# Performance work log

Hardware: AMD Instinct MI355X
Metric: run time of the kernel (lower is better)

The kernel has to match this reference:

```python
import jax, jax.numpy as jnp
import numpy as np

N = 6144; D0 = 512; D1 = 256; D2 = 128; K = 10
ALPHA = 1.0; BETA = 1.0; P = 0.004  # edge density -> ~25 avg degree


def _xavier(key, shape):
    limit = float(np.sqrt(6.0 / (shape[0] + shape[1])))
    return jax.random.uniform(key, shape, jnp.float32, -limit, limit)


def setup_inputs() -> dict:
    key = jax.random.key(0)
    ks = jax.random.split(key, 20)

    def adj(k):
        k1, k2 = jax.random.split(k)
        u = jax.random.uniform(k1, (N, N), jnp.float32)
        w = jax.random.uniform(k2, (N, N), jnp.float32)
        return jnp.where(u < P, w, 0.0)  # sparse weighted adjacency, dense storage

    return {
        "A": adj(ks[0]), "A2": adj(ks[1]),
        "X": jax.random.normal(ks[2], (N, D0), jnp.float32),
        "X2": jax.random.normal(ks[3], (N, D0), jnp.float32),
        "W11": _xavier(ks[4], (D0, D1)), "v111": _xavier(ks[5], (D1, 1)), "v112": _xavier(ks[6], (D1, 1)),
        "W12": _xavier(ks[7], (D1, D2)), "v121": _xavier(ks[8], (D2, 1)), "v122": _xavier(ks[9], (D2, 1)),
        "W21": _xavier(ks[10], (D0, D1)), "v211": _xavier(ks[11], (D1, 1)), "v212": _xavier(ks[12], (D1, 1)),
        "W22": _xavier(ks[13], (D1, D2)), "v221": _xavier(ks[14], (D2, 1)), "v222": _xavier(ks[15], (D2, 1)),
        "mu": _xavier(ks[16], (K, D2)),
    }


def _gat(A, H, v1, v2):
    # logits_ij = A_ij * (H v1)_i + A_ij * (H v2)_j, support = nonzeros of A;
    # torch.sparse.softmax over each row of sigmoid(logits) restricted to support.
    f1 = H @ v1                       # [N,1]
    f2 = H @ v2                       # [N,1]
    logits = A * f1 + A * f2.T        # [N,N]
    mask = A != 0.0
    e = jnp.where(mask, jnp.exp(jax.nn.sigmoid(logits)), 0.0)
    denom = jnp.sum(e, axis=1, keepdims=True)
    return e / jnp.where(denom == 0.0, 1.0, denom)  # empty rows -> all-zero row


def _autoenc(A, X, layers):
    H = X
    Cs = []
    for (W, v1, v2) in layers:          # encoder
        H = H @ W
        C = _gat(A, H, v1, v2)
        Cs.append(C)
        H = C @ H
    H_enc = H
    for i in range(len(layers) - 1, -1, -1):  # decoder (tied weights, cached attention)
        H = H @ layers[i][0].T
        H = Cs[i] @ H
    return H_enc, H


def reference(A, X, A2, X2, W11, v111, v112, W12, v121, v122,
              W21, v211, v212, W22, v221, v222, mu):
    H, X_ = _autoenc(A, X, [(W11, v111, v112), (W12, v121, v122)])
    H2, X_2 = _autoenc(A2, X2, [(W21, v211, v212), (W22, v221, v222)])
    H_F = H + H2 * BETA
    # Student-t soft assignment
    d2 = jnp.sum((H_F[:, None, :] - mu[None, :, :]) ** 2, axis=2)  # [N,K]
    q = (1.0 / (1.0 + d2 / ALPHA)) ** ((ALPHA + 1.0) / 2.0)
    q = q / jnp.sum(q, axis=1, keepdims=True)
    return (H_F, q, H, H2, X_, X_2)
```

## Files before the change

kernel.cpp:

```cpp
#include <hip/hip_runtime.h>
#include <hip/hip_bf16.h>

#define NN 6144
#define CAP 128

typedef short bf8 __attribute__((ext_vector_type(8)));
typedef float f4 __attribute__((ext_vector_type(4)));

__device__ inline unsigned short f2bf(float x) {
  union { float f; unsigned u; } v; v.f = x;
  unsigned r = v.u + 0x7fff + ((v.u >> 16) & 1);
  return (unsigned short)(r >> 16);
}
__device__ inline float bf2f(unsigned short b) {
  union { float f; unsigned u; } v; v.u = ((unsigned)b) << 16;
  return v.f;
}


__device__ void dev_sparsify(int bid, int tid,
    const float* __restrict__ A0, const float* __restrict__ A1,
    int* __restrict__ colsB, float* __restrict__ valsB, int* __restrict__ cntB) {
  const int br = bid >= 1536;
  const int bb = br ? bid - 1536 : bid;
  const float* __restrict__ A = br ? A1 : A0;
  int* cols = colsB + (size_t)br * NN * CAP;
  float* vals = valsB + (size_t)br * NN * CAP;
  int* cnt = cntB + br * NN;
  int row = (bb * 256 + tid) >> 6;
  int lane = tid & 63;
  const f4* __restrict__ arow = (const f4*)(A + (size_t)row * NN);
  int base = 0;
  for (int it = 0; it < 24; it += 6) {
    f4 v[6];
#pragma unroll
    for (int u = 0; u < 6; ++u) v[u] = __builtin_nontemporal_load(&arow[(it + u) * 64 + lane]);
#pragma unroll
    for (int u = 0; u < 6; ++u) {
      float xs[4] = {v[u][0], v[u][1], v[u][2], v[u][3]};
      unsigned long long m[4];
#pragma unroll
      for (int q = 0; q < 4; ++q) m[q] = __ballot(xs[q] != 0.0f);
      int off0 = base;
      int off1 = off0 + __popcll(m[0]);
      int off2 = off1 + __popcll(m[1]);
      int off3 = off2 + __popcll(m[2]);
      base = off3 + __popcll(m[3]);
      int offs[4] = {off0, off1, off2, off3};
      unsigned long long lmask = (1ull << lane) - 1ull;
#pragma unroll
      for (int q = 0; q < 4; ++q) {
        if (xs[q] != 0.0f) {
          int idx = offs[q] + __popcll(m[q] & lmask);
          if (idx < CAP) {
            cols[row * CAP + idx] = ((it + u) * 64 + lane) * 4 + q;
            vals[row * CAP + idx] = xs[q];
          }
        }
      }
    }
  }
  if (lane == 0) cnt[row] = base < CAP ? base : CAP;
}

__device__ void dev_convw(int cb, int tid,
    const float* __restrict__ W11, const float* __restrict__ W21,
    const float* __restrict__ W12, const float* __restrict__ W22,
    short* __restrict__ W1th, short* __restrict__ W1tl,
    short* __restrict__ W2th, short* __restrict__ W2tl) {
  const int S1 = 512 * 256, S2 = 256 * 128;
  int i = cb * 256 + tid;
  if (i < 2 * S1) {
    int br = i >= S1;
    int idx = br ? i - S1 : i;
    float x = (br ? W21 : W11)[idx];
    unsigned short h = f2bf(x), l = f2bf(x - bf2f(h));
    int r = idx / 256, c = idx % 256;
    size_t o = (size_t)br * S1;
    W1th[o + c * 512 + r] = (short)h; W1tl[o + c * 512 + r] = (short)l;
  } else {
    int i2 = i - 2 * S1;
    if (i2 >= 2 * S2) return;
    int br = i2 >= S2;
    int idx = br ? i2 - S2 : i2;
    float x = (br ? W22 : W12)[idx];
    unsigned short h = f2bf(x), l = f2bf(x - bf2f(h));
    int r = idx / 128, c = idx % 128;
    size_t o = (size_t)br * S2;
    W2th[o + c * 256 + r] = (short)h; W2tl[o + c * 256 + r] = (short)l;
  }
}

__device__ void dev_convX(int xb, int tid,
    const float* __restrict__ X0, const float* __restrict__ X1,
    short* __restrict__ XhB) {
  const int br = xb >= 3072;
  const int b = br ? xb - 3072 : xb;
  const float* __restrict__ in = br ? X1 : X0;
  short* hi = XhB + (size_t)br * NN * 512;
  int i = b * 256 + tid;
  float4 v = *(const float4*)&in[i * 4];
  short4 h;
  h.x = (short)f2bf(v.x);
  h.y = (short)f2bf(v.y);
  h.z = (short)f2bf(v.z);
  h.w = (short)f2bf(v.w);
  *(short4*)&hi[i * 4] = h;
}

__device__ void dev_wc2(int wb, int tid, char* smemc,
    const float* __restrict__ W11, const float* __restrict__ W12,
    const float* __restrict__ W21, const float* __restrict__ W22,
    short* __restrict__ Wch, short* __restrict__ Wcl) {
  const int bx = wb & 7, by = (wb >> 3) & 1, br = wb >> 4;
  const float* W1 = br ? W21 : W11;
  const float* W2 = br ? W22 : W12;
  short* Ch = Wch + (size_t)br * 512 * 128;
  short* Cl = Wcl + (size_t)br * 512 * 128;
  float (*As)[68] = (float(*)[68])smemc;
  float (*Bs)[68] = (float(*)[68])(smemc + 16 * 68 * 4);
  const int bm = bx * 64, bn = by * 64;
  const int t = tid;
  const int tm = (t >> 4) * 4, tn = (t & 15) * 4;
  const int la_m = t >> 2, la_k = (t & 3) * 4;
  const int lb_k = t >> 4, lb_n = (t & 15) * 4;
  float acc[4][4] = {};
  for (int k0 = 0; k0 < 256; k0 += 16) {
    float4 a4 = *(const float4*)&W1[(size_t)(bm + la_m) * 256 + k0 + la_k];
    float4 b4 = *(const float4*)&W2[(size_t)(k0 + lb_k) * 128 + bn + lb_n];
    __syncthreads();
    As[la_k + 0][la_m] = a4.x;
    As[la_k + 1][la_m] = a4.y;
    As[la_k + 2][la_m] = a4.z;
    As[la_k + 3][la_m] = a4.w;
    Bs[lb_k][lb_n + 0] = b4.x;
    Bs[lb_k][lb_n + 1] = b4.y;
    Bs[lb_k][lb_n + 2] = b4.z;
    Bs[lb_k][lb_n + 3] = b4.w;
    __syncthreads();
#pragma unroll
    for (int k = 0; k < 16; ++k) {
      float a0 = As[k][tm + 0], a1 = As[k][tm + 1], a2 = As[k][tm + 2], a3 = As[k][tm + 3];
      float b0 = Bs[k][tn + 0], b1 = Bs[k][tn + 1], b2 = Bs[k][tn + 2], b3 = Bs[k][tn + 3];
      acc[0][0] += a0 * b0; acc[0][1] += a0 * b1; acc[0][2] += a0 * b2; acc[0][3] += a0 * b3;
      acc[1][0] += a1 * b0; acc[1][1] += a1 * b1; acc[1][2] += a1 * b2; acc[1][3] += a1 * b3;
      acc[2][0] += a2 * b0; acc[2][1] += a2 * b1; acc[2][2] += a2 * b2; acc[2][3] += a2 * b3;
      acc[3][0] += a3 * b0; acc[3][1] += a3 * b1; acc[3][2] += a3 * b2; acc[3][3] += a3 * b3;
    }
  }
#pragma unroll
  for (int i = 0; i < 4; ++i)
#pragma unroll
    for (int j = 0; j < 4; ++j) {
      float x = acc[i][j];
      size_t off = (size_t)(bm + tm + i) * 128 + bn + tn + j;
      unsigned short h = f2bf(x);
      Ch[off] = (short)h;
      Cl[off] = (short)f2bf(x - bf2f(h));
    }
}

__device__ void dev_fvec256(int fb, int tid,
    const short* __restrict__ HB, const float* __restrict__ v10,
    const float* __restrict__ v20, const float* __restrict__ v11,
    const float* __restrict__ v21, float* __restrict__ f1B, float* __restrict__ f2B) {
  const int br = fb >= 1536;
  const int bb = br ? fb - 1536 : fb;
  const short* H = HB + (size_t)br * NN * 256;
  const float* v1 = br ? v11 : v10;
  const float* v2 = br ? v21 : v20;
  float* f1 = f1B + br * NN;
  float* f2 = f2B + br * NN;
  int row = (bb * 256 + tid) >> 6;
  int lane = tid & 63;
  const short* hp = H + (size_t)row * 256 + lane * 4;
  float s1 = 0.f, s2 = 0.f;
#pragma unroll
  for (int e = 0; e < 4; ++e) {
    float h = bf2f((unsigned short)hp[e]);
    s1 += h * v1[lane * 4 + e];
    s2 += h * v2[lane * 4 + e];
  }
#pragma unroll
  for (int o = 32; o; o >>= 1) {
    s1 += __shfl_xor(s1, o);
    s2 += __shfl_xor(s2, o);
  }
  if (lane == 0) { f1[row] = s1; f2[row] = s2; }
}

#define GS 40
#define MFMA_BF16 __builtin_amdgcn_mfma_f32_16x16x32_bf16

template <bool ALO, int EPI>
__device__ void dev_gemm(int bx, int by, int br, int tid, char* smemc,
    const short* __restrict__ AhB, const short* __restrict__ AlB, size_t sA,
    const short* __restrict__ BhB, const short* __restrict__ BlB, size_t sB,
    float* __restrict__ CfB, short* __restrict__ ChB, short* __restrict__ ClB,
    size_t sC, int K, int Nn) {
  short* sAh = (short*)smemc;
  short* sBh = sAh + 64 * GS;
  short* sBl = sBh + 64 * GS;
  short* sAl = sBl + 64 * GS;
  const short* Ahg = AhB + br * sA;
  const short* Bhg = BhB + br * sB;
  const short* Blg = BlB + br * sB;
  const int bm = bx * 64, bn = by * 64;
  const int t = tid;
  const int lane = t & 63, w = t >> 6;
  const int wm = (w & 1) * 32, wn = (w >> 1) * 32;
  const int fr = lane & 15, fq = lane >> 4;
  const int srow = t >> 2, sk = (t & 3) * 8;

  f4 acc[2][2] = {};

  for (int k0 = 0; k0 < K; k0 += 32) {
    const size_t aoff = (size_t)(bm + srow) * K + k0 + sk;
    const size_t boff = (size_t)(bn + srow) * K + k0 + sk;
    bf8 vah = *(const bf8*)&Ahg[aoff];
    bf8 vbh = *(const bf8*)&Bhg[boff];
    bf8 vbl = *(const bf8*)&Blg[boff];
    bf8 val_;
    if constexpr (ALO) val_ = *(const bf8*)&(AlB + br * sA)[aoff];
    __syncthreads();
    *(bf8*)&sAh[srow * GS + sk] = vah;
    *(bf8*)&sBh[srow * GS + sk] = vbh;
    *(bf8*)&sBl[srow * GS + sk] = vbl;
    if constexpr (ALO) *(bf8*)&sAl[srow * GS + sk] = val_;
    __syncthreads();

    bf8 ah[2], al[2], bh[2], bl[2];
#pragma unroll
    for (int i = 0; i < 2; ++i) {
      ah[i] = *(bf8*)&sAh[(wm + i * 16 + fr) * GS + fq * 8];
      bh[i] = *(bf8*)&sBh[(wn + i * 16 + fr) * GS + fq * 8];
      bl[i] = *(bf8*)&sBl[(wn + i * 16 + fr) * GS + fq * 8];
      if constexpr (ALO) al[i] = *(bf8*)&sAl[(wm + i * 16 + fr) * GS + fq * 8];
    }
#pragma unroll
    for (int mi = 0; mi < 2; ++mi)
#pragma unroll
      for (int ni = 0; ni < 2; ++ni) {
        acc[mi][ni] = MFMA_BF16(ah[mi], bh[ni], acc[mi][ni], 0, 0, 0);
        acc[mi][ni] = MFMA_BF16(ah[mi], bl[ni], acc[mi][ni], 0, 0, 0);
        if constexpr (ALO) acc[mi][ni] = MFMA_BF16(al[mi], bh[ni], acc[mi][ni], 0, 0, 0);
      }
  }

  float* Cf = CfB ? CfB + br * sC : nullptr;
  short* Ch = ChB ? ChB + br * sC : nullptr;
  short* Cl = ClB ? ClB + br * sC : nullptr;
#pragma unroll
  for (int mi = 0; mi < 2; ++mi)
#pragma unroll
    for (int ni = 0; ni < 2; ++ni) {
      int cidx = bn + wn + ni * 16 + fr;
#pragma unroll
      for (int r = 0; r < 4; ++r) {
        size_t off = (size_t)(bm + wm + mi * 16 + fq * 4 + r) * Nn + cidx;
        float x = acc[mi][ni][r];
        if constexpr (EPI == 0) Cf[off] = x;
        if constexpr (EPI >= 1) {
          unsigned short h = f2bf(x);
          Ch[off] = (short)h;
          if constexpr (EPI == 2) Cl[off] = (short)f2bf(x - bf2f(h));
        }
      }
    }
}

template <bool WLO>
__device__ void dev_spmm128(int sb, int tid,
    const int* __restrict__ colsB, const float* __restrict__ cvalsB,
    const int* __restrict__ cntB, const short* __restrict__ HinB,
    short* __restrict__ HhB, short* __restrict__ HlB) {
  const int br = sb >= 1536;
  const int bb = br ? sb - 1536 : sb;
  const int* cols = colsB + (size_t)br * NN * CAP;
  const float* cvals = cvalsB + (size_t)br * NN * CAP;
  const int* cnt = cntB + br * NN;
  const short* Hin = HinB + (size_t)br * NN * 128;
  int row = (bb * 256 + tid) >> 6;
  int lane = tid & 63;
  int c = cnt[row];
  const int base = row * CAP;
  float cv0 = 0.f, cv1 = 0.f;
  int j0 = 0, j1 = 0;
  if (lane < c) { j0 = cols[base + lane]; cv0 = cvals[base + lane]; }
  if (64 + lane < c) { j1 = cols[base + 64 + lane]; cv1 = cvals[base + 64 + lane]; }
  float2 acc = make_float2(0.f, 0.f);
  for (int k = 0; k < c; k += 8) {
    unsigned hv[8]; float cv[8];
#pragma unroll
    for (int u = 0; u < 8; ++u) {
      int kk = k + u;
      if (kk < c) {
        int jj = (kk & 64) ? j1 : j0;
        float cc = (kk & 64) ? cv1 : cv0;
        int j = __shfl(jj, kk & 63);
        cv[u] = __shfl(cc, kk & 63);
        hv[u] = *(const unsigned*)&Hin[(size_t)j * 128 + lane * 2];
      }
    }
#pragma unroll
    for (int u = 0; u < 8; ++u) {
      if (k + u < c) {
        acc.x += cv[u] * bf2f((unsigned short)(hv[u] & 0xffff));
        acc.y += cv[u] * bf2f((unsigned short)(hv[u] >> 16));
      }
    }
  }
  size_t o = (size_t)br * NN * 128 + (size_t)row * 128 + lane * 2;
  unsigned short hx = f2bf(acc.x), hy = f2bf(acc.y);
  *(unsigned*)&HhB[o] = (unsigned)hx | ((unsigned)hy << 16);
  if constexpr (WLO) {
    unsigned short lx = f2bf(acc.x - bf2f(hx)), ly = f2bf(acc.y - bf2f(hy));
    *(unsigned*)&HlB[o] = (unsigned)lx | ((unsigned)ly << 16);
  }
}

__device__ void dev_final(int fb, int tid,
    const float* __restrict__ H1e, const float* __restrict__ H2e,
    const float* __restrict__ mu, float* __restrict__ hf_out,
    float* __restrict__ q_out) {
  int row = (fb * 256 + tid) >> 6;
  int lane = tid & 63;
  float2 h1 = *(const float2*)&H1e[row * 128 + lane * 2];
  float2 h2 = *(const float2*)&H2e[row * 128 + lane * 2];
  float2 hf = make_float2(h1.x + h2.x, h1.y + h2.y);
  *(float2*)&hf_out[row * 128 + lane * 2] = hf;
  float d2[10];
#pragma unroll
  for (int k = 0; k < 10; ++k) {
    float dx = hf.x - mu[k * 128 + lane * 2];
    float dy = hf.y - mu[k * 128 + lane * 2 + 1];
    d2[k] = dx * dx + dy * dy;
  }
#pragma unroll
  for (int k = 0; k < 10; ++k)
#pragma unroll
    for (int o = 32; o; o >>= 1) d2[k] += __shfl_xor(d2[k], o);
  float q[10], s = 0.f;
#pragma unroll
  for (int k = 0; k < 10; ++k) { q[k] = 1.f / (1.f + d2[k]); s += q[k]; }
  float inv = 1.f / s;
  if (lane < 10) q_out[row * 10 + lane] = q[lane] * inv;
}


__global__ __launch_bounds__(256) void k1_prep(
    const float* A0, const float* A1, int* colsB, float* valsB, int* cntB,
    const float* W11, const float* W21, const float* W12, const float* W22,
    short* W1th, short* W1tl, short* W2th, short* W2tl,
    const float* X0, const float* X1, short* XhB,
    short* Wc2h, short* Wc2l) {
  __shared__ char smem[2 * 16 * 68 * 4];
  int bid = blockIdx.x, tid = threadIdx.x;
  if (bid < 3072) dev_sparsify(bid, tid, A0, A1, colsB, valsB, cntB);
  else if (bid < 4352) dev_convw(bid - 3072, tid, W11, W21, W12, W22,
                                 W1th, W1tl, W2th, W2tl);
  else if (bid < 10496) dev_convX(bid - 4352, tid, X0, X1, XhB);
  else dev_wc2(bid - 10496, tid, smem, W11, W12, W21, W22, Wc2h, Wc2l);
}

template <bool ALO, int EPI>
__global__ __launch_bounds__(256) void gemm_nt(
    const short* AhB, const short* AlB, size_t sA,
    const short* BhB, const short* BlB, size_t sB,
    float* CfB, short* ChB, short* ClB, size_t sC, int K, int Nn) {
  __shared__ char smem[(ALO ? 4 : 3) * 64 * GS * 2];
  dev_gemm<ALO, EPI>(blockIdx.x, blockIdx.y, blockIdx.z, threadIdx.x, smem,
                     AhB, AlB, sA, BhB, BlB, sB, CfB, ChB, ClB, sC, K, Nn);
}

__global__ __launch_bounds__(256) void k3_gemm2_fvec(
    const short* H1h, const short* W2th, const short* W2tl, short* G1h,
    const float* v111, const float* v112, const float* v211, const float* v212,
    float* f1, float* f2) {
  __shared__ char smem[3 * 64 * GS * 2];
  int bid = blockIdx.x, tid = threadIdx.x;
  if (bid < 384) {
    int bx = bid % 96, r = bid / 96;
    int by = r & 1, br = r >> 1;
    dev_gemm<false, 1>(bx, by, br, tid, smem, H1h, nullptr, (size_t)NN * 256,
                       W2th, W2tl, (size_t)256 * 128, nullptr, G1h, nullptr,
                       (size_t)NN * 128, 256, 128);
  } else {
    dev_fvec256(bid - 384, tid, H1h, v111, v112, v211, v212, f1, f2);
  }
}

template <bool WF32, bool FUSE>
__global__ __launch_bounds__(256) void gatspmm_kernel(
    const int* __restrict__ colsB, const float* __restrict__ avalsB,
    const int* __restrict__ cntB, const float* __restrict__ f1B,
    const float* __restrict__ f2B, float* __restrict__ cvalsB,
    const short* __restrict__ HinB, float* __restrict__ HoutB,
    short* __restrict__ HhB,
    const float* __restrict__ nv10, const float* __restrict__ nv20,
    const float* __restrict__ nv11, const float* __restrict__ nv21,
    float* __restrict__ g1B, float* __restrict__ g2B) {
  const int br = blockIdx.y;
  const int* cols = colsB + (size_t)br * NN * CAP;
  const float* avals = avalsB + (size_t)br * NN * CAP;
  const int* cnt = cntB + br * NN;
  const float* f1 = f1B + br * NN;
  const float* f2 = f2B + br * NN;
  float* cvals = cvalsB + (size_t)br * NN * CAP;
  const short* Hin = HinB + (size_t)br * NN * 128;
  int row = (blockIdx.x * blockDim.x + threadIdx.x) >> 6;
  int lane = threadIdx.x & 63;
  int c = cnt[row];
  float f1i = f1[row];
  const int base = row * CAP;
  float e0 = 0.f, e1 = 0.f;
  int j0 = 0, j1 = 0;
  {
    int k = lane;
    if (k < c) {
      float a = avals[base + k];
      j0 = cols[base + k];
      float lg = a * (f1i + f2[j0]);
      e0 = expf(1.f / (1.f + expf(-lg)));
    }
    k = 64 + lane;
    if (k < c) {
      float a = avals[base + k];
      j1 = cols[base + k];
      float lg = a * (f1i + f2[j1]);
      e1 = expf(1.f / (1.f + expf(-lg)));
    }
  }
  float s = e0 + e1;
#pragma unroll
  for (int o = 32; o; o >>= 1) s += __shfl_xor(s, o);
  float inv = (s == 0.f) ? 1.f : 1.f / s;
  if (lane < c) cvals[base + lane] = e0 * inv;
  if (64 + lane < c) cvals[base + 64 + lane] = e1 * inv;

  float2 acc = make_float2(0.f, 0.f);
  for (int k = 0; k < c; k += 8) {
    unsigned hv[8]; float cv[8];
#pragma unroll
    for (int u = 0; u < 8; ++u) {
      int kk = k + u;
      if (kk < c) {
        int jj = (kk & 64) ? j1 : j0;
        float ee = (kk & 64) ? e1 : e0;
        int j = __shfl(jj, kk & 63);
        cv[u] = __shfl(ee, kk & 63) * inv;
        hv[u] = *(const unsigned*)&Hin[(size_t)j * 128 + lane * 2];
      }
    }
#pragma unroll
    for (int u = 0; u < 8; ++u) {
      if (k + u < c) {
        acc.x += cv[u] * bf2f((unsigned short)(hv[u] & 0xffff));
        acc.y += cv[u] * bf2f((unsigned short)(hv[u] >> 16));
      }
    }
  }
  size_t o = (size_t)br * NN * 128 + (size_t)row * 128 + lane * 2;
  if constexpr (WF32) *(float2*)&HoutB[o] = acc;
  unsigned hw = (unsigned)(unsigned short)f2bf(acc.x) | ((unsigned)f2bf(acc.y) << 16);
  *(unsigned*)&HhB[o] = hw;
  if constexpr (FUSE) {
    const float* w1 = br ? nv11 : nv10;
    const float* w2 = br ? nv21 : nv20;
    float s1 = acc.x * w1[lane * 2] + acc.y * w1[lane * 2 + 1];
    float s2 = acc.x * w2[lane * 2] + acc.y * w2[lane * 2 + 1];
#pragma unroll
    for (int o2 = 32; o2; o2 >>= 1) {
      s1 += __shfl_xor(s1, o2);
      s2 += __shfl_xor(s2, o2);
    }
    if (lane == 0) { g1B[br * NN + row] = s1; g2B[br * NN + row] = s2; }
  }
}

__global__ __launch_bounds__(256) void k6_spmm_final(
    const int* colsB, const float* c2v, const int* cntB,
    const short* Hech, short* C2sh,
    const float* H1e, const float* H2e, const float* mu,
    float* hf_out, float* q_out) {
  int bid = blockIdx.x, tid = threadIdx.x;
  if (bid < 3072) dev_spmm128<false>(bid, tid, colsB, c2v, cntB, Hech, C2sh, nullptr);
  else dev_final(bid - 3072, tid, H1e, H2e, mu, hf_out, q_out);
}

__global__ __launch_bounds__(256) void spmm128hl_kernel(
    const int* colsB, const float* cvalsB, const int* cntB,
    const short* HinB, short* HhB, short* HlB) {
  dev_spmm128<true>(blockIdx.x + blockIdx.y * 1536, threadIdx.x,
                    colsB, cvalsB, cntB, HinB, HhB, HlB);
}

extern "C" void kernel_launch(void* const* d_in, const int* in_sizes, int n_in,
                              void* d_out, int out_size, void* d_ws, size_t ws_size,
                              hipStream_t stream) {
  const int D0 = 512, D1 = 256, D2 = 128;
  const int S1 = D0 * D1, S2 = D1 * D2;
  float* out = (float*)d_out;
  const size_t o0 = 0;
  const size_t o1 = o0 + (size_t)NN * 128;
  const size_t o2 = o1 + (size_t)NN * 10;
  const size_t o3 = o2 + (size_t)NN * 128;
  const size_t o4 = o3 + (size_t)NN * 128;
  const size_t o5 = o4 + (size_t)NN * 512;

  char* w = (char*)d_ws;
  auto alloc = [&](size_t bytes) -> void* {
    void* p = (void*)w;
    w += (bytes + 255) & ~(size_t)255;
    return p;
  };
  int*   cols  = (int*)  alloc((size_t)2 * NN * CAP * 4);
  float* avals = (float*)alloc((size_t)2 * NN * CAP * 4);
  float* c1v   = (float*)alloc((size_t)2 * NN * CAP * 4);
  float* c2v   = (float*)alloc((size_t)2 * NN * CAP * 4);
  int*   cnt   = (int*)  alloc((size_t)2 * NN * 4);
  float* f1    = (float*)alloc((size_t)2 * NN * 4);
  float* f2    = (float*)alloc((size_t)2 * NN * 4);
  float* g1    = (float*)alloc((size_t)2 * NN * 4);
  float* g2    = (float*)alloc((size_t)2 * NN * 4);
  short* Xh    = (short*)alloc((size_t)2 * NN * D0 * 2);
  short* H1h   = (short*)alloc((size_t)2 * NN * D1 * 2);
  short* G1h   = (short*)alloc((size_t)2 * NN * D2 * 2);
  short* H2h   = (short*)alloc((size_t)2 * NN * D2 * 2);
  short* Hech  = (short*)alloc((size_t)2 * NN * D2 * 2);
  short* C2sh  = (short*)alloc((size_t)2 * NN * D2 * 2);
  short* Cth   = (short*)alloc((size_t)2 * NN * D2 * 2);
  short* Ctl   = (short*)alloc((size_t)2 * NN * D2 * 2);
  short* W1th  = (short*)alloc((size_t)2 * S1 * 2);
  short* W1tl  = (short*)alloc((size_t)2 * S1 * 2);
  short* W2th  = (short*)alloc((size_t)2 * S2 * 2);
  short* W2tl  = (short*)alloc((size_t)2 * S2 * 2);
  short* Wc2h  = (short*)alloc((size_t)2 * 512 * 128 * 2);
  short* Wc2l  = (short*)alloc((size_t)2 * 512 * 128 * 2);

  const float* A   = (const float*)d_in[0];
  const float* A2  = (const float*)d_in[1];
  const float* X   = (const float*)d_in[2];
  const float* X2  = (const float*)d_in[3];
  const float* W11 = (const float*)d_in[4];
  const float* v111= (const float*)d_in[5];
  const float* v112= (const float*)d_in[6];
  const float* W12 = (const float*)d_in[7];
  const float* v121= (const float*)d_in[8];
  const float* v122= (const float*)d_in[9];
  const float* W21 = (const float*)d_in[10];
  const float* v211= (const float*)d_in[11];
  const float* v212= (const float*)d_in[12];
  const float* W22 = (const float*)d_in[13];
  const float* v221= (const float*)d_in[14];
  const float* v222= (const float*)d_in[15];
  const float* mu  = (const float*)d_in[16];

  const dim3 rows2(NN / 4, 2);

  k1_prep<<<10528, 256, 0, stream>>>(
      A, A2, cols, avals, cnt, W11, W21, W12, W22,
      W1th, W1tl, W2th, W2tl, X, X2, Xh, Wc2h, Wc2l);
  gemm_nt<false, 1><<<dim3(NN / 64, D1 / 64, 2), 256, 0, stream>>>(
      Xh, nullptr, (size_t)NN * D0, W1th, W1tl, (size_t)S1,
      nullptr, H1h, nullptr, (size_t)NN * D1, D0, D1);
  k3_gemm2_fvec<<<3456, 256, 0, stream>>>(
      H1h, W2th, W2tl, G1h, v111, v112, v211, v212, f1, f2);
  gatspmm_kernel<false, true><<<rows2, 256, 0, stream>>>(
      cols, avals, cnt, f1, f2, c1v, G1h, nullptr, H2h,
      v121, v122, v221, v222, g1, g2);
  gatspmm_kernel<true, false><<<rows2, 256, 0, stream>>>(
      cols, avals, cnt, g1, g2, c2v, H2h, out + o2, Hech,
      nullptr, nullptr, nullptr, nullptr, nullptr, nullptr);
  k6_spmm_final<<<4608, 256, 0, stream>>>(
      cols, c2v, cnt, Hech, C2sh, out + o2, out + o3, mu, out + o0, out + o1);
  spmm128hl_kernel<<<rows2, 256, 0, stream>>>(cols, c1v, cnt, C2sh, Cth, Ctl);
  gemm_nt<true, 0><<<dim3(NN / 64, D0 / 64, 2), 256, 0, stream>>>(
      Cth, Ctl, (size_t)NN * D2, Wc2h, Wc2l, (size_t)(512 * 128),
      out + o4, nullptr, nullptr, (size_t)NN * D0, D2, D0);
}
```

Before: 164.3 us.

## Overlap adjacency sparsification with first GEMM and stage CSR writes via LDS

Splits the prep kernel in two. The W/X bf16 conversions run first. A second kernel then runs the adjacency sparsification, the first feature GEMM (X·W1) and the Wc2 construction as separate block ranges, so the bandwidth-bound scan of A can overlap with the compute-bound GEMM. Sparsify now builds each row's column and value lists in shared memory and writes all CAP slots with coalesced stores, replacing scattered per-lane global writes. The trade-offs are one extra launch and the copying of stale or uninitialized staging entries past each row's count into global memory.

```diff
diff --git a/kernel.cpp b/kernel.cpp
--- a/kernel.cpp
+++ b/kernel.cpp
@@ -18,7 +18,7 @@
 }
 
 
-__device__ void dev_sparsify(int bid, int tid,
+__device__ void dev_sparsify(int bid, int tid, char* smem,
     const float* __restrict__ A0, const float* __restrict__ A1,
     int* __restrict__ colsB, float* __restrict__ valsB, int* __restrict__ cntB) {
   const int br = bid >= 1536;
@@ -27,8 +27,10 @@
   int* cols = colsB + (size_t)br * NN * CAP;
   float* vals = valsB + (size_t)br * NN * CAP;
   int* cnt = cntB + br * NN;
-  int row = (bb * 256 + tid) >> 6;
-  int lane = tid & 63;
+  const int wv = tid >> 6, lane = tid & 63;
+  const int row = bb * 4 + wv;
+  int* colstage = (int*)(smem + wv * 1024);
+  float* valstage = (float*)(smem + wv * 1024 + 512);
   const f4* __restrict__ arow = (const f4*)(A + (size_t)row * NN);
   int base = 0;
   for (int it = 0; it < 24; it += 6) {
@@ -53,13 +55,21 @@
         if (xs[q] != 0.0f) {
           int idx = offs[q] + __popcll(m[q] & lmask);
           if (idx < CAP) {
-            cols[row * CAP + idx] = ((it + u) * 64 + lane) * 4 + q;
-            vals[row * CAP + idx] = xs[q];
+            colstage[idx] = ((it + u) * 64 + lane) * 4 + q;
+            valstage[idx] = xs[q];
           }
         }
       }
     }
   }
+  __syncthreads();
+  const int rbase = row * CAP;
+  int c0 = colstage[lane], c1 = colstage[64 + lane];
+  float v0 = valstage[lane], v1 = valstage[64 + lane];
+  cols[rbase + lane] = c0;
+  cols[rbase + 64 + lane] = c1;
+  vals[rbase + lane] = v0;
+  vals[rbase + 64 + lane] = v1;
   if (lane == 0) cnt[row] = base < CAP ? base : CAP;
 }
 
@@ -348,19 +358,34 @@
 }
 
 
-__global__ __launch_bounds__(256) void k1_prep(
-    const float* A0, const float* A1, int* colsB, float* valsB, int* cntB,
+__global__ __launch_bounds__(256) void k0_prep(
     const float* W11, const float* W21, const float* W12, const float* W22,
     short* W1th, short* W1tl, short* W2th, short* W2tl,
-    const float* X0, const float* X1, short* XhB,
+    const float* X0, const float* X1, short* XhB) {
+  int bid = blockIdx.x, tid = threadIdx.x;
+  if (bid < 1280) dev_convw(bid, tid, W11, W21, W12, W22, W1th, W1tl, W2th, W2tl);
+  else dev_convX(bid - 1280, tid, X0, X1, XhB);
+}
+
+__global__ __launch_bounds__(256) void k1_main(
+    const float* A0, const float* A1, int* colsB, float* valsB, int* cntB,
+    const short* Xh, const short* W1th, const short* W1tl, short* H1h,
+    const float* W11, const float* W12, const float* W21, const float* W22,
     short* Wc2h, short* Wc2l) {
-  __shared__ char smem[2 * 16 * 68 * 4];
+  __shared__ char smem[15360];
   int bid = blockIdx.x, tid = threadIdx.x;
-  if (bid < 3072) dev_sparsify(bid, tid, A0, A1, colsB, valsB, cntB);
-  else if (bid < 4352) dev_convw(bid - 3072, tid, W11, W21, W12, W22,
-                                 W1th, W1tl, W2th, W2tl);
-  else if (bid < 10496) dev_convX(bid - 4352, tid, X0, X1, XhB);
-  else dev_wc2(bid - 10496, tid, smem, W11, W12, W21, W22, Wc2h, Wc2l);
+  if (bid < 3072) {
+    dev_sparsify(bid, tid, smem, A0, A1, colsB, valsB, cntB);
+  } else if (bid < 3840) {
+    int g = bid - 3072;
+    int bx = g % 96, r = g / 96;
+    int by = r & 3, brz = r >> 2;
+    dev_gemm<false, 1>(bx, by, brz, tid, smem, Xh, nullptr, (size_t)NN * 512,
+                       W1th, W1tl, (size_t)512 * 256, nullptr, H1h, nullptr,
+                       (size_t)NN * 256, 512, 256);
+  } else {
+    dev_wc2(bid - 3840, tid, smem, W11, W12, W21, W22, Wc2h, Wc2l);
+  }
 }
 
 template <bool ALO, int EPI>
@@ -558,12 +583,11 @@
 
   const dim3 rows2(NN / 4, 2);
 
-  k1_prep<<<10528, 256, 0, stream>>>(
-      A, A2, cols, avals, cnt, W11, W21, W12, W22,
-      W1th, W1tl, W2th, W2tl, X, X2, Xh, Wc2h, Wc2l);
-  gemm_nt<false, 1><<<dim3(NN / 64, D1 / 64, 2), 256, 0, stream>>>(
-      Xh, nullptr, (size_t)NN * D0, W1th, W1tl, (size_t)S1,
-      nullptr, H1h, nullptr, (size_t)NN * D1, D0, D1);
+  k0_prep<<<7424, 256, 0, stream>>>(
+      W11, W21, W12, W22, W1th, W1tl, W2th, W2tl, X, X2, Xh);
+  k1_main<<<3872, 256, 0, stream>>>(
+      A, A2, cols, avals, cnt, Xh, W1th, W1tl, H1h,
+      W11, W12, W21, W22, Wc2h, Wc2l);
   k3_gemm2_fvec<<<3456, 256, 0, stream>>>(
       H1h, W2th, W2tl, G1h, v111, v112, v211, v212, f1, f2);
   gatspmm_kernel<false, true><<<rows2, 256, 0, stream>>>(
```

Result: no change. 163.4 us (-0.5%).
